# Kernel optimization log

Hardware: AMD Instinct MI355X
Metric: run time of the kernel (lower is better)

The kernel has to match this reference:

```python
import jax, jax.numpy as jnp
import numpy as np

EPS = 1e-6
NEG = -1e9
RES_RATIO = 1.0  # res_ratio init arg
MAKE_SYM = True


def _ln(x, g, b):
    m = jnp.mean(x, axis=-1, keepdims=True)
    v = jnp.mean((x - m) ** 2, axis=-1, keepdims=True)
    return (x - m) * jax.lax.rsqrt(v + EPS) * g + b


def _sim(q, k, W1q, W1k, b1, W2, b2):
    # NN(concat([q,k])) with first dense split into query/key halves:
    # relu(q@W1q + k@W1k + b1) @ W2 + b2  -> avoids materializing the 2d concat.
    qa = q @ W1q  # [b,n,sq,h]
    kb = k @ W1k  # [b,n,sk,h]
    h1 = jax.nn.relu(qa[:, :, :, None, :] + kb[:, :, None, :, :] + b1)  # [b,n,sq,sk,h]
    s = jnp.einsum('bnqkh,h->bnqk', h1, W2[:, 0]) + b2[0]
    if MAKE_SYM:
        qb = q @ W1k
        ka = k @ W1q
        h2 = jax.nn.relu(ka[:, :, None, :, :] + qb[:, :, :, None, :] + b1)
        s = s + jnp.einsum('bnqkh,h->bnqk', h2, W2[:, 0]) + b2[0]
    return s


def _attention(v, k, q, mask, Ww, bw, Wd, bd, W1q, W1k, b1, W2, b2):
    q = q @ Ww + bw
    k = k @ Ww + bw
    v = v @ Ww + bw
    logits = _sim(q, k, W1q, W1k, b1, W2, b2)
    if mask is not None:
        logits = logits + mask * NEG
    attn = jax.nn.softmax(logits, axis=-1)
    out = jnp.einsum('bnqk,bnkd->bnqd', attn, v)
    return out @ Wd + bd, attn


def setup_inputs() -> dict:
    key = jax.random.key(0)
    B, N, S, D, DFF, H = 4, 1, 256, 128, 512, 128
    ks = jax.random.split(key, 16)
    s = 0.02
    inp = {
        'x': jax.random.normal(ks[0], (B, N, S, D), jnp.float32),
        'enc_output': jax.random.normal(ks[1], (B, N, S, D), jnp.float32),
        'com_mask': jnp.zeros((B, N, S, S), jnp.float32),
        'dec_mask': jnp.zeros((B, N, S, S), jnp.float32),
        # shared pairwise-score MLP NN: Dense(H, relu) -> Dense(1)
        'W1q': jax.random.normal(ks[2], (D, H), jnp.float32) * s,
        'W1k': jax.random.normal(ks[3], (D, H), jnp.float32) * s,
        'b1': jnp.zeros((H,), jnp.float32),
        'W2': jax.random.normal(ks[4], (H, 1), jnp.float32) * s,
        'b2': jnp.zeros((1,), jnp.float32),
        # mha1 projections
        'Ww1': jax.random.normal(ks[5], (D, D), jnp.float32) * s,
        'bw1': jnp.zeros((D,), jnp.float32),
        'Wd1': jax.random.normal(ks[6], (D, D), jnp.float32) * s,
        'bd1': jnp.zeros((D,), jnp.float32),
        # mha2 projections
        'Ww2': jax.random.normal(ks[7], (D, D), jnp.float32) * s,
        'bw2': jnp.zeros((D,), jnp.float32),
        'Wd2': jax.random.normal(ks[8], (D, D), jnp.float32) * s,
        'bd2': jnp.zeros((D,), jnp.float32),
        # ffn
        'Wf1': jax.random.normal(ks[9], (D, DFF), jnp.float32) * s,
        'bf1': jnp.zeros((DFF,), jnp.float32),
        'Wf2': jax.random.normal(ks[10], (DFF, D), jnp.float32) * s,
        'bf2': jnp.zeros((D,), jnp.float32),
        # layernorms
        'ln1_g': jnp.ones((D,), jnp.float32), 'ln1_b': jnp.zeros((D,), jnp.float32),
        'ln2_g': jnp.ones((D,), jnp.float32), 'ln2_b': jnp.zeros((D,), jnp.float32),
        'ln3_g': jnp.ones((D,), jnp.float32), 'ln3_b': jnp.zeros((D,), jnp.float32),
    }
    return inp


def reference(x, enc_output, com_mask, dec_mask,
              W1q, W1k, b1, W2, b2,
              Ww1, bw1, Wd1, bd1,
              Ww2, bw2, Wd2, bd2,
              Wf1, bf1, Wf2, bf2,
              ln1_g, ln1_b, ln2_g, ln2_b, ln3_g, ln3_b):
    r = RES_RATIO
    # self-attention block (dropout inactive, eval mode)
    attn1, aw1 = _attention(x, x, x, com_mask, Ww1, bw1, Wd1, bd1, W1q, W1k, b1, W2, b2)
    out1 = _ln((2 - r) * attn1 + r * x, ln1_g, ln1_b)
    # cross-attention block
    attn2, aw2 = _attention(enc_output, enc_output, out1, dec_mask, Ww2, bw2, Wd2, bd2, W1q, W1k, b1, W2, b2)
    out2 = _ln((2 - r) * attn2 + r * out1, ln2_g, ln2_b)
    # ffn
    ffn = jax.nn.relu(out2 @ Wf1 + bf1) @ Wf2 + bf2
    out3 = _ln((2 - r) * ffn + r * out2, ln3_g, ln3_b)
    return out3
```

## Files before the change

kernel.cpp:

```cpp
#include <hip/hip_runtime.h>
#include <math.h>


#define LN_EPS 1e-6f
#define NEGV  (-1e9f)

constexpr int B = 4, S = 256, D = 128, H = 128, DFF = 512;
constexpr int R = B * S;

struct P {
    const float *x, *enc, *com_mask, *dec_mask;
    const float *W1q, *W1k, *b1, *W2;
    const float *Ww1, *bw1, *Wd1, *bd1;
    const float *Ww2, *bw2, *Wd2, *bd2;
    const float *Wf1, *bf1, *Wf2, *bf2;
    const float *ln1g, *ln1b, *ln2g, *ln2b, *ln3g, *ln3b;
    float *out;
    float *xw, *qa, *kb, *kv2w, *kb2, *ka2;
};

__global__ __launch_bounds__(512) void proj3_kernel(P p)
{
    const int g = blockIdx.y, tid = threadIdx.x;
    const int r0 = blockIdx.x * 8;
    __shared__ __align__(16) float Ash[8 * 128];
    __shared__ __align__(16) float Pw[8 * 128];
    __shared__ __align__(16) float Pp[2 * 8 * 128];

    const float* A    = g ? p.enc  : p.x;
    const float* Wp   = g ? p.Ww2  : p.Ww1;
    const float* bp   = g ? p.bw2  : p.bw1;
    float*       o_w  = g ? p.kv2w : p.xw;
    const float* Wsec = g ? p.W1k  : p.W1q;
    const float* bsec = g ? nullptr: p.b1;
    float*       o_s  = g ? p.kb2  : p.qa;
    const float* Wthr = g ? p.W1q  : p.W1k;
    float*       o_t  = g ? p.ka2  : p.kb;

    if (tid < 256)
        ((float4*)Ash)[tid] = ((const float4*)(A + (size_t)r0 * 128))[tid];
    __syncthreads();

    {
        const int kh = tid >> 8, unit = tid & 255, lr = unit >> 5, c4 = unit & 31;
        const float4* W4 = (const float4*)Wp;
        float4 acc = (kh == 0) ? ((const float4*)bp)[c4] : make_float4(0.f, 0.f, 0.f, 0.f);
        const int k0 = kh * 64;
        #pragma unroll 8
        for (int k = 0; k < 64; ++k) {
            const float a = Ash[lr * 128 + k0 + k];
            const float4 w = W4[(k0 + k) * 32 + c4];
            acc.x = fmaf(a, w.x, acc.x); acc.y = fmaf(a, w.y, acc.y);
            acc.z = fmaf(a, w.z, acc.z); acc.w = fmaf(a, w.w, acc.w);
        }
        ((float4*)Pp)[kh * 256 + unit] = acc;
    }
    __syncthreads();
    if (tid < 256) {
        const int lr = tid >> 5, c4 = tid & 31;
        const float4 a = ((const float4*)Pp)[tid];
        const float4 bq = ((const float4*)Pp)[256 + tid];
        const float4 w = make_float4(a.x + bq.x, a.y + bq.y, a.z + bq.z, a.w + bq.w);
        ((float4*)Pw)[tid] = w;
        ((float4*)o_w)[(size_t)(r0 + lr) * 32 + c4] = w;
    }
    __syncthreads();

    {
        const int which = tid >> 8, unit = tid & 255, lr = unit >> 5, c4 = unit & 31;
        const float* W = which ? Wthr : Wsec;
        const float* bb = which ? nullptr : bsec;
        float* o = which ? o_t : o_s;
        const float4* W4 = (const float4*)W;
        float4 acc = bb ? ((const float4*)bb)[c4] : make_float4(0.f, 0.f, 0.f, 0.f);
        #pragma unroll 8
        for (int k = 0; k < 128; ++k) {
            const float a = Pw[lr * 128 + k];
            const float4 w = W4[k * 32 + c4];
            acc.x = fmaf(a, w.x, acc.x); acc.y = fmaf(a, w.y, acc.y);
            acc.z = fmaf(a, w.z, acc.z); acc.w = fmaf(a, w.w, acc.w);
        }
        ((float4*)o)[(size_t)(r0 + lr) * 32 + c4] = acc;
    }
}

#define SC8(ACC, O1, X1, O2, X2)                                               \
    ACC = fmaf(fmaxf((O1).x + (X1).x, 0.f), w.x, ACC);                         \
    ACC = fmaf(fmaxf((O1).y + (X1).y, 0.f), w.y, ACC);                         \
    ACC = fmaf(fmaxf((O1).z + (X1).z, 0.f), w.z, ACC);                         \
    ACC = fmaf(fmaxf((O1).w + (X1).w, 0.f), w.w, ACC);                         \
    ACC = fmaf(fmaxf((O2).x + (X2).x, 0.f), w.x, ACC);                         \
    ACC = fmaf(fmaxf((O2).y + (X2).y, 0.f), w.y, ACC);                         \
    ACC = fmaf(fmaxf((O2).z + (X2).z, 0.f), w.z, ACC);                         \
    ACC = fmaf(fmaxf((O2).w + (X2).w, 0.f), w.w, ACC);

template<bool FIRST>
__device__ __forceinline__ void attn_stage(const P& p, float* smem,
                                           int tid, int r0, int bS)
{
    float* s8   = smem;
    float* rowS = smem + 1024;
    float* qa2L = smem + 18432;
    float* qb2L = smem + 18944;

    const float* __restrict__ S1g = FIRST ? p.kb : p.kb2;
    const float* __restrict__ S2g = FIRST ? p.qa : p.ka2;
    const float* mask = FIRST ? p.com_mask : p.dec_mask;
    const float* V    = FIRST ? p.xw : p.kv2w;
    const float* Wd   = FIRST ? p.Wd1 : p.Wd2;
    const float* bd   = FIRST ? p.bd1 : p.bd2;
    const float* lg   = FIRST ? p.ln1g : p.ln2g;
    const float* lb   = FIRST ? p.ln1b : p.ln2b;

    {
        const int hh = tid & 7, unit = tid >> 3, kk = unit & 31, rg = unit >> 5;
        const int rA = r0 + 2 * rg, rB = rA + 1;

        float4 o1A[4], o1B[4], o2A[4], o2B[4], w2r[4];
        #pragma unroll
        for (int j = 0; j < 4; ++j) {
            const int h = hh * 4 + 32 * j;
            if (FIRST) {
                o1A[j] = *(const float4*)(p.qa + (size_t)rA * H + h);
                o1B[j] = *(const float4*)(p.qa + (size_t)rB * H + h);
                o2A[j] = *(const float4*)(p.kb + (size_t)rA * H + h);
                o2B[j] = *(const float4*)(p.kb + (size_t)rB * H + h);
            } else {
                o1A[j] = *(const float4*)(qa2L + (2 * rg)     * H + h);
                o1B[j] = *(const float4*)(qa2L + (2 * rg + 1) * H + h);
                o2A[j] = *(const float4*)(qb2L + (2 * rg)     * H + h);
                o2B[j] = *(const float4*)(qb2L + (2 * rg + 1) * H + h);
            }
            w2r[j] = *(const float4*)(p.W2 + h);
        }

        for (int kt = 0; kt < 4; ++kt) {
            const float* __restrict__ r1a = S1g + (size_t)(bS + kt * 64 + kk)      * H;
            const float* __restrict__ r1b = S1g + (size_t)(bS + kt * 64 + kk + 32) * H;
            const float* __restrict__ r2a = S2g + (size_t)(bS + kt * 64 + kk)      * H;
            const float* __restrict__ r2b = S2g + (size_t)(bS + kt * 64 + kk + 32) * H;

            float4 x1a[4], x1b[4], x2a[4], x2b[4];
            #pragma unroll
            for (int j = 0; j < 4; ++j) {
                const int h = hh * 4 + 32 * j;
                x1a[j] = *(const float4*)(r1a + h);
                x1b[j] = *(const float4*)(r1b + h);
                x2a[j] = *(const float4*)(r2a + h);
                x2b[j] = *(const float4*)(r2b + h);
            }

            float aAa = 0.f, aAb = 0.f, aBa = 0.f, aBb = 0.f;
            #pragma unroll
            for (int j = 0; j < 4; ++j) {
                const float4 w = w2r[j];
                SC8(aAa, o1A[j], x1a[j], o2A[j], x2a[j])
                SC8(aAb, o1A[j], x1b[j], o2A[j], x2b[j])
                SC8(aBa, o1B[j], x1a[j], o2B[j], x2a[j])
                SC8(aBb, o1B[j], x1b[j], o2B[j], x2b[j])
            }
            #pragma unroll
            for (int o = 1; o < 8; o <<= 1) {
                aAa += __shfl_xor(aAa, o, 8);
                aAb += __shfl_xor(aAb, o, 8);
                aBa += __shfl_xor(aBa, o, 8);
                aBb += __shfl_xor(aBb, o, 8);
            }
            if (hh == 0) {
                const int kb0 = kt * 64;
                s8[(2 * rg)     * 256 + kb0 + kk]      = aAa;
                s8[(2 * rg)     * 256 + kb0 + kk + 32] = aAb;
                s8[(2 * rg + 1) * 256 + kb0 + kk]      = aBa;
                s8[(2 * rg + 1) * 256 + kb0 + kk + 32] = aBb;
            }
        }
    }
    __syncthreads();

    for (int i = tid; i < 1024; i += 512) {
        const int r = i >> 8, k = i & 255;
        s8[i] += mask[(size_t)(r0 + r) * S + k] * NEGV;
    }
    __syncthreads();

    {
        const int g = tid >> 6, c = tid & 63;
        if (g < 4) {
            float* rowp = s8 + g * 256;
            float m = -INFINITY;
            #pragma unroll
            for (int k = c; k < 256; k += 64) m = fmaxf(m, rowp[k]);
            for (int o = 32; o; o >>= 1) m = fmaxf(m, __shfl_xor(m, o, 64));
            float s = 0.f;
            #pragma unroll
            for (int k = c; k < 256; k += 64) { const float e = __expf(rowp[k] - m); rowp[k] = e; s += e; }
            for (int o = 32; o; o >>= 1) s += __shfl_xor(s, o, 64);
            const float rinv = 1.f / s;
            #pragma unroll
            for (int k = c; k < 256; k += 64) rowp[k] *= rinv;
        }
    }
    __syncthreads();

    float* avp = smem + 1536;
    float* aoS = smem + 3584;
    float* pp  = smem + 4096;

    {
        const int r = tid >> 7, t = tid & 127, kq = t >> 5, c4 = t & 31;
        const float4* V4 = (const float4*)(V + (size_t)bS * D);
        const float* sp = s8 + r * 256 + kq * 64;
        float4 acc = make_float4(0.f, 0.f, 0.f, 0.f);
        #pragma unroll 8
        for (int k = 0; k < 64; ++k) {
            const float a = sp[k];
            const float4 v = V4[(kq * 64 + k) * 32 + c4];
            acc.x = fmaf(a, v.x, acc.x); acc.y = fmaf(a, v.y, acc.y);
            acc.z = fmaf(a, v.z, acc.z); acc.w = fmaf(a, v.w, acc.w);
        }
        ((float4*)avp)[(r * 4 + kq) * 32 + c4] = acc;
    }
    __syncthreads();
    if (tid < 128) {
        const int r = tid >> 5, c4 = tid & 31;
        float4 s0 = ((const float4*)avp)[(r * 4 + 0) * 32 + c4];
        const float4 s1 = ((const float4*)avp)[(r * 4 + 1) * 32 + c4];
        const float4 s2 = ((const float4*)avp)[(r * 4 + 2) * 32 + c4];
        const float4 s3 = ((const float4*)avp)[(r * 4 + 3) * 32 + c4];
        s0.x += s1.x + s2.x + s3.x; s0.y += s1.y + s2.y + s3.y;
        s0.z += s1.z + s2.z + s3.z; s0.w += s1.w + s2.w + s3.w;
        ((float4*)aoS)[r * 32 + c4] = s0;
    }
    __syncthreads();

    {
        const int kq = tid >> 7, unit = tid & 127, r = unit >> 5, c4 = unit & 31;
        const float4* W4 = (const float4*)Wd;
        const float* ap = aoS + r * 128 + kq * 32;
        float4 acc = make_float4(0.f, 0.f, 0.f, 0.f);
        #pragma unroll 8
        for (int k = 0; k < 32; ++k) {
            const float a = ap[k];
            const float4 w = W4[(kq * 32 + k) * 32 + c4];
            acc.x = fmaf(a, w.x, acc.x); acc.y = fmaf(a, w.y, acc.y);
            acc.z = fmaf(a, w.z, acc.z); acc.w = fmaf(a, w.w, acc.w);
        }
        ((float4*)pp)[kq * 128 + unit] = acc;
    }
    __syncthreads();

    if (tid < 128) {
        const int r = tid >> 5, c4 = tid & 31;
        const float4 p0 = ((const float4*)pp)[tid];
        const float4 p1 = ((const float4*)pp)[128 + tid];
        const float4 p2 = ((const float4*)pp)[256 + tid];
        const float4 p3 = ((const float4*)pp)[384 + tid];
        const float4 bv0 = ((const float4*)bd)[c4];
        float4 r4;
        if (FIRST) r4 = ((const float4*)(p.x + (size_t)(r0 + r) * 128))[c4];
        else       r4 = ((const float4*)rowS)[r * 32 + c4];
        const float x0 = p0.x + p1.x + p2.x + p3.x + bv0.x + r4.x;
        const float x1 = p0.y + p1.y + p2.y + p3.y + bv0.y + r4.y;
        const float x2 = p0.z + p1.z + p2.z + p3.z + bv0.z + r4.z;
        const float x3 = p0.w + p1.w + p2.w + p3.w + bv0.w + r4.w;
        float s  = x0 + x1 + x2 + x3;
        float s2 = x0 * x0 + x1 * x1 + x2 * x2 + x3 * x3;
        for (int o = 16; o; o >>= 1) { s += __shfl_xor(s, o, 32); s2 += __shfl_xor(s2, o, 32); }
        const float m = s * (1.f / 128), var = s2 * (1.f / 128) - m * m;
        const float rs = rsqrtf(var + LN_EPS);
        const float4 gv = ((const float4*)lg)[c4], bv = ((const float4*)lb)[c4];
        float4 o4;
        o4.x = (x0 - m) * rs * gv.x + bv.x; o4.y = (x1 - m) * rs * gv.y + bv.y;
        o4.z = (x2 - m) * rs * gv.z + bv.z; o4.w = (x3 - m) * rs * gv.w + bv.w;
        ((float4*)rowS)[r * 32 + c4] = o4;
    }
    __syncthreads();

    if (FIRST) {
        float* qpp  = smem + 6144;
        float* q2wS = smem + 8192;
        float* qp2  = smem + 8704;
        {
            const int kq = tid >> 7, unit = tid & 127, r = unit >> 5, c4 = unit & 31;
            const float4* W4 = (const float4*)p.Ww2;
            const float* ap = rowS + r * 128 + kq * 32;
            float4 acc = make_float4(0.f, 0.f, 0.f, 0.f);
            #pragma unroll 8
            for (int k = 0; k < 32; ++k) {
                const float a = ap[k];
                const float4 w = W4[(kq * 32 + k) * 32 + c4];
                acc.x = fmaf(a, w.x, acc.x); acc.y = fmaf(a, w.y, acc.y);
                acc.z = fmaf(a, w.z, acc.z); acc.w = fmaf(a, w.w, acc.w);
            }
            ((float4*)qpp)[kq * 128 + unit] = acc;
        }
        __syncthreads();
        if (tid < 128) {
            const int c4 = tid & 31;
            const float4 p0 = ((const float4*)qpp)[tid];
            const float4 p1 = ((const float4*)qpp)[128 + tid];
            const float4 p2 = ((const float4*)qpp)[256 + tid];
            const float4 p3 = ((const float4*)qpp)[384 + tid];
            const float4 bw = ((const float4*)p.bw2)[c4];
            ((float4*)q2wS)[tid] = make_float4(p0.x + p1.x + p2.x + p3.x + bw.x,
                                               p0.y + p1.y + p2.y + p3.y + bw.y,
                                               p0.z + p1.z + p2.z + p3.z + bw.z,
                                               p0.w + p1.w + p2.w + p3.w + bw.w);
        }
        __syncthreads();
        {
            const int which = tid >> 8, sub = tid & 255;
            const int kh = sub >> 7, unit2 = sub & 127;
            const float4* W4 = (const float4*)(which ? p.W1k : p.W1q);
            const int r = unit2 >> 5;
            const float* ap = q2wS + r * 128 + kh * 64;
            float4 acc = make_float4(0.f, 0.f, 0.f, 0.f);
            #pragma unroll 8
            for (int k = 0; k < 64; ++k) {
                const float a = ap[k];
                const float4 w = W4[(kh * 64 + k) * 32 + (unit2 & 31)];
                acc.x = fmaf(a, w.x, acc.x); acc.y = fmaf(a, w.y, acc.y);
                acc.z = fmaf(a, w.z, acc.z); acc.w = fmaf(a, w.w, acc.w);
            }
            ((float4*)qp2)[(which * 2 + kh) * 128 + unit2] = acc;
        }
        __syncthreads();
        if (tid < 256) {
            const int which = tid >> 7, unit2 = tid & 127;
            const int c4 = unit2 & 31;
            const float4 p0 = ((const float4*)qp2)[(which * 2 + 0) * 128 + unit2];
            const float4 p1 = ((const float4*)qp2)[(which * 2 + 1) * 128 + unit2];
            const float4 b1v = ((const float4*)p.b1)[c4];
            float* oq = which ? qb2L : qa2L;
            ((float4*)oq)[unit2] =
                make_float4(p0.x + p1.x + b1v.x, p0.y + p1.y + b1v.y,
                            p0.z + p1.z + b1v.z, p0.w + p1.w + b1v.w);
        }
        __syncthreads();
    } else {
        float* hidP = smem + 1536;
        float* part = smem + 9984;
        {
            const int c = tid & 127, kh = tid >> 7;
            const float4* Wf1_4 = (const float4*)p.Wf1;
            float4 a0 = make_float4(0.f,0.f,0.f,0.f), a1 = a0, a2 = a0, a3 = a0;
            const int kbase = kh * 32;
            #pragma unroll 8
            for (int k = 0; k < 32; ++k) {
                const int kk = kbase + k;
                const float4 w = Wf1_4[kk * 128 + c];
                const float s0 = rowS[kk],       s1 = rowS[128 + kk];
                const float s2 = rowS[256 + kk], s3 = rowS[384 + kk];
                a0.x=fmaf(s0,w.x,a0.x); a0.y=fmaf(s0,w.y,a0.y); a0.z=fmaf(s0,w.z,a0.z); a0.w=fmaf(s0,w.w,a0.w);
                a1.x=fmaf(s1,w.x,a1.x); a1.y=fmaf(s1,w.y,a1.y); a1.z=fmaf(s1,w.z,a1.z); a1.w=fmaf(s1,w.w,a1.w);
                a2.x=fmaf(s2,w.x,a2.x); a2.y=fmaf(s2,w.y,a2.y); a2.z=fmaf(s2,w.z,a2.z); a2.w=fmaf(s2,w.w,a2.w);
                a3.x=fmaf(s3,w.x,a3.x); a3.y=fmaf(s3,w.y,a3.y); a3.z=fmaf(s3,w.z,a3.z); a3.w=fmaf(s3,w.w,a3.w);
            }
            float4* h4 = (float4*)hidP;
            const int base = kh * 512;
            h4[base + 0*128 + c] = a0; h4[base + 1*128 + c] = a1;
            h4[base + 2*128 + c] = a2; h4[base + 3*128 + c] = a3;
        }
        __syncthreads();
        for (int i = tid; i < 2048; i += 512) {
            hidP[i] = fmaxf(hidP[i] + hidP[2048 + i] + hidP[4096 + i] + hidP[6144 + i]
                            + p.bf1[i & 511], 0.f);
        }
        __syncthreads();
        {
            const int c4f = tid & 31, kg = tid >> 5;
            const float4* Wf2_4 = (const float4*)p.Wf2;
            float4 a0 = make_float4(0.f,0.f,0.f,0.f), a1 = a0, a2 = a0, a3 = a0;
            const int kbase = kg * 32;
            const float* h0 = hidP + 0 * 512 + kbase;
            const float* h1 = hidP + 1 * 512 + kbase;
            const float* h2 = hidP + 2 * 512 + kbase;
            const float* h3 = hidP + 3 * 512 + kbase;
            #pragma unroll 8
            for (int k = 0; k < 32; ++k) {
                const float4 w = Wf2_4[(kbase + k) * 32 + c4f];
                const float s0 = h0[k], s1 = h1[k], s2 = h2[k], s3 = h3[k];
                a0.x=fmaf(s0,w.x,a0.x); a0.y=fmaf(s0,w.y,a0.y); a0.z=fmaf(s0,w.z,a0.z); a0.w=fmaf(s0,w.w,a0.w);
                a1.x=fmaf(s1,w.x,a1.x); a1.y=fmaf(s1,w.y,a1.y); a1.z=fmaf(s1,w.z,a1.z); a1.w=fmaf(s1,w.w,a1.w);
                a2.x=fmaf(s2,w.x,a2.x); a2.y=fmaf(s2,w.y,a2.y); a2.z=fmaf(s2,w.z,a2.z); a2.w=fmaf(s2,w.w,a2.w);
                a3.x=fmaf(s3,w.x,a3.x); a3.y=fmaf(s3,w.y,a3.y); a3.z=fmaf(s3,w.z,a3.z); a3.w=fmaf(s3,w.w,a3.w);
            }
            float4* p4 = (float4*)part;
            p4[kg * 128 + 0 * 32 + c4f] = a0; p4[kg * 128 + 1 * 32 + c4f] = a1;
            p4[kg * 128 + 2 * 32 + c4f] = a2; p4[kg * 128 + 3 * 32 + c4f] = a3;
        }
        __syncthreads();
        if (tid < 128) {
            const int r = tid >> 5, c4 = tid & 31;
            const float4* p4 = (const float4*)part;
            float4 sum = ((const float4*)p.bf2)[c4];
            #pragma unroll
            for (int kg = 0; kg < 16; ++kg) {
                const float4 v = p4[kg * 128 + r * 32 + c4];
                sum.x += v.x; sum.y += v.y; sum.z += v.z; sum.w += v.w;
            }
            const float4 r4 = ((const float4*)rowS)[r * 32 + c4];
            const float x0 = sum.x + r4.x, x1 = sum.y + r4.y;
            const float x2 = sum.z + r4.z, x3 = sum.w + r4.w;
            float s  = x0 + x1 + x2 + x3;
            float s2 = x0 * x0 + x1 * x1 + x2 * x2 + x3 * x3;
            for (int o = 16; o; o >>= 1) { s += __shfl_xor(s, o, 32); s2 += __shfl_xor(s2, o, 32); }
            const float m = s * (1.f / 128), var = s2 * (1.f / 128) - m * m;
            const float rs = rsqrtf(var + LN_EPS);
            const float4 gv = ((const float4*)p.ln3g)[c4], bv = ((const float4*)p.ln3b)[c4];
            float4 o4;
            o4.x = (x0 - m) * rs * gv.x + bv.x; o4.y = (x1 - m) * rs * gv.y + bv.y;
            o4.z = (x2 - m) * rs * gv.z + bv.z; o4.w = (x3 - m) * rs * gv.w + bv.w;
            ((float4*)p.out)[(size_t)(r0 + r) * 32 + c4] = o4;
        }
    }
}

__global__ __launch_bounds__(512) void fused_attn12_kernel(P p)
{
    __shared__ __align__(16) float smem[19456];
    const int tid = threadIdx.x;
    const int r0 = blockIdx.x * 4, bS = (r0 >> 8) * S;
    attn_stage<true >(p, smem, tid, r0, bS);
    attn_stage<false>(p, smem, tid, r0, bS);
}

extern "C" void kernel_launch(void* const* d_in, const int* in_sizes, int n_in,
                              void* d_out, int out_size, void* d_ws, size_t ws_size,
                              hipStream_t stream) {
    (void)in_sizes; (void)n_in; (void)out_size; (void)ws_size;
    P p;
    p.x        = (const float*)d_in[0];
    p.enc      = (const float*)d_in[1];
    p.com_mask = (const float*)d_in[2];
    p.dec_mask = (const float*)d_in[3];
    p.W1q = (const float*)d_in[4];
    p.W1k = (const float*)d_in[5];
    p.b1  = (const float*)d_in[6];
    p.W2  = (const float*)d_in[7];
    p.Ww1 = (const float*)d_in[9];
    p.bw1 = (const float*)d_in[10];
    p.Wd1 = (const float*)d_in[11];
    p.bd1 = (const float*)d_in[12];
    p.Ww2 = (const float*)d_in[13];
    p.bw2 = (const float*)d_in[14];
    p.Wd2 = (const float*)d_in[15];
    p.bd2 = (const float*)d_in[16];
    p.Wf1 = (const float*)d_in[17];
    p.bf1 = (const float*)d_in[18];
    p.Wf2 = (const float*)d_in[19];
    p.bf2 = (const float*)d_in[20];
    p.ln1g = (const float*)d_in[21];
    p.ln1b = (const float*)d_in[22];
    p.ln2g = (const float*)d_in[23];
    p.ln2b = (const float*)d_in[24];
    p.ln3g = (const float*)d_in[25];
    p.ln3b = (const float*)d_in[26];
    p.out  = (float*)d_out;

    float* ws = (float*)d_ws;
    const size_t RD = (size_t)R * D;
    p.xw    = ws;
    p.qa    = p.xw    + RD;
    p.kb    = p.qa    + RD;
    p.kv2w  = p.kb    + RD;
    p.kb2   = p.kv2w  + RD;
    p.ka2   = p.kb2   + RD;

    proj3_kernel<<<dim3(R / 8, 2), 512, 0, stream>>>(p);
    fused_attn12_kernel<<<R / 4, 512, 0, stream>>>(p);
}
```

Before: 164.5 us.

## Split projection K-loops, double-buffer key loads, fold mask and softmax normalization

The projection kernel now handles 4 rows per block with a 4-way and then a 2-way split-K and shared-memory reductions, so it launches twice as many blocks and each thread runs a shorter serial loop. In the attention stage, key-side rows are double-buffered in registers so the next tile's global loads are issued while the current tile is being computed. The mask add moves into the score write, which removes one pass over shared memory and a barrier. Softmax normalization is deferred to the attention-output reduction through a per-row reciprocal, and the shared-memory layout is compacted. The cost is more registers for the double buffers and extra barriers in the projection kernel.

```diff
diff --git a/kernel.cpp b/kernel.cpp
--- a/kernel.cpp
+++ b/kernel.cpp
@@ -22,10 +22,11 @@
 __global__ __launch_bounds__(512) void proj3_kernel(P p)
 {
     const int g = blockIdx.y, tid = threadIdx.x;
-    const int r0 = blockIdx.x * 8;
-    __shared__ __align__(16) float Ash[8 * 128];
-    __shared__ __align__(16) float Pw[8 * 128];
-    __shared__ __align__(16) float Pp[2 * 8 * 128];
+    const int r0 = blockIdx.x * 4;
+    __shared__ __align__(16) float Ash[4 * 128];
+    __shared__ __align__(16) float Pw[4 * 128];
+    __shared__ __align__(16) float Pp[4 * 4 * 128];
+    __shared__ __align__(16) float P2[2 * 2 * 4 * 128];
 
     const float* A    = g ? p.enc  : p.x;
     const float* Wp   = g ? p.Ww2  : p.Ww1;
@@ -37,50 +38,67 @@
     const float* Wthr = g ? p.W1q  : p.W1k;
     float*       o_t  = g ? p.ka2  : p.kb;
 
-    if (tid < 256)
+    if (tid < 128)
         ((float4*)Ash)[tid] = ((const float4*)(A + (size_t)r0 * 128))[tid];
     __syncthreads();
 
     {
-        const int kh = tid >> 8, unit = tid & 255, lr = unit >> 5, c4 = unit & 31;
+        const int kh = tid >> 7, unit = tid & 127, lr = unit >> 5, c4 = unit & 31;
         const float4* W4 = (const float4*)Wp;
         float4 acc = (kh == 0) ? ((const float4*)bp)[c4] : make_float4(0.f, 0.f, 0.f, 0.f);
-        const int k0 = kh * 64;
+        const int k0 = kh * 32;
         #pragma unroll 8
-        for (int k = 0; k < 64; ++k) {
+        for (int k = 0; k < 32; ++k) {
             const float a = Ash[lr * 128 + k0 + k];
             const float4 w = W4[(k0 + k) * 32 + c4];
             acc.x = fmaf(a, w.x, acc.x); acc.y = fmaf(a, w.y, acc.y);
             acc.z = fmaf(a, w.z, acc.z); acc.w = fmaf(a, w.w, acc.w);
         }
-        ((float4*)Pp)[kh * 256 + unit] = acc;
-    }
-    __syncthreads();
-    if (tid < 256) {
+        ((float4*)Pp)[kh * 128 + unit] = acc;
+    }
+    __syncthreads();
+    if (tid < 128) {
         const int lr = tid >> 5, c4 = tid & 31;
-        const float4 a = ((const float4*)Pp)[tid];
-        const float4 bq = ((const float4*)Pp)[256 + tid];
-        const float4 w = make_float4(a.x + bq.x, a.y + bq.y, a.z + bq.z, a.w + bq.w);
+        const float4 a0 = ((const float4*)Pp)[tid];
+        const float4 a1 = ((const float4*)Pp)[128 + tid];
+        const float4 a2 = ((const float4*)Pp)[256 + tid];
+        const float4 a3 = ((const float4*)Pp)[384 + tid];
+        const float4 w = make_float4(a0.x + a1.x + a2.x + a3.x,
+                                     a0.y + a1.y + a2.y + a3.y,
+                                     a0.z + a1.z + a2.z + a3.z,
+                                     a0.w + a1.w + a2.w + a3.w);
         ((float4*)Pw)[tid] = w;
         ((float4*)o_w)[(size_t)(r0 + lr) * 32 + c4] = w;
     }
     __syncthreads();
 
     {
-        const int which = tid >> 8, unit = tid & 255, lr = unit >> 5, c4 = unit & 31;
+        const int which = tid >> 8, sub = tid & 255;
+        const int kh = sub >> 7, unit2 = sub & 127, lr = unit2 >> 5, c4 = unit2 & 31;
         const float* W = which ? Wthr : Wsec;
         const float* bb = which ? nullptr : bsec;
-        float* o = which ? o_t : o_s;
         const float4* W4 = (const float4*)W;
-        float4 acc = bb ? ((const float4*)bb)[c4] : make_float4(0.f, 0.f, 0.f, 0.f);
+        float4 acc = (kh == 0 && bb) ? ((const float4*)bb)[c4]
+                                     : make_float4(0.f, 0.f, 0.f, 0.f);
+        const int k0 = kh * 64;
         #pragma unroll 8
-        for (int k = 0; k < 128; ++k) {
-            const float a = Pw[lr * 128 + k];
-            const float4 w = W4[k * 32 + c4];
+        for (int k = 0; k < 64; ++k) {
+            const float a = Pw[lr * 128 + k0 + k];
+            const float4 w = W4[(k0 + k) * 32 + c4];
             acc.x = fmaf(a, w.x, acc.x); acc.y = fmaf(a, w.y, acc.y);
             acc.z = fmaf(a, w.z, acc.z); acc.w = fmaf(a, w.w, acc.w);
         }
-        ((float4*)o)[(size_t)(r0 + lr) * 32 + c4] = acc;
+        ((float4*)P2)[(which * 2 + kh) * 128 + unit2] = acc;
+    }
+    __syncthreads();
+    if (tid < 256) {
+        const int which = tid >> 7, unit2 = tid & 127;
+        const int lr = unit2 >> 5, c4 = unit2 & 31;
+        const float4 p0 = ((const float4*)P2)[(which * 2 + 0) * 128 + unit2];
+        const float4 p1 = ((const float4*)P2)[(which * 2 + 1) * 128 + unit2];
+        float* o = which ? o_t : o_s;
+        ((float4*)o)[(size_t)(r0 + lr) * 32 + c4] =
+            make_float4(p0.x + p1.x, p0.y + p1.y, p0.z + p1.z, p0.w + p1.w);
     }
 }
 
@@ -94,14 +112,32 @@
     ACC = fmaf(fmaxf((O2).z + (X2).z, 0.f), w.z, ACC);                         \
     ACC = fmaf(fmaxf((O2).w + (X2).w, 0.f), w.w, ACC);
 
+#define LOADK(BUF, KT)                                                         \
+    {                                                                          \
+        const float* r1a_ = S1g + (size_t)(bS + (KT) * 64 + kk) * H;           \
+        const float* r1b_ = S1g + (size_t)(bS + (KT) * 64 + kk + 32) * H;      \
+        const float* r2a_ = S2g + (size_t)(bS + (KT) * 64 + kk) * H;           \
+        const float* r2b_ = S2g + (size_t)(bS + (KT) * 64 + kk + 32) * H;      \
+        _Pragma("unroll")                                                      \
+        for (int j = 0; j < 4; ++j) {                                          \
+            const int h = hh * 4 + 32 * j;                                     \
+            X1a[BUF][j] = *(const float4*)(r1a_ + h);                          \
+            X1b[BUF][j] = *(const float4*)(r1b_ + h);                          \
+            X2a[BUF][j] = *(const float4*)(r2a_ + h);                          \
+            X2b[BUF][j] = *(const float4*)(r2b_ + h);                          \
+        }                                                                      \
+    }
+
 template<bool FIRST>
 __device__ __forceinline__ void attn_stage(const P& p, float* smem,
                                            int tid, int r0, int bS)
 {
-    float* s8   = smem;
-    float* rowS = smem + 1024;
-    float* qa2L = smem + 18432;
-    float* qb2L = smem + 18944;
+    float* s8    = smem;
+    float* rowS  = smem + 1024;
+    float* rinvS = smem + 1536;
+    float* qa2L  = smem + 1552;
+    float* qb2L  = smem + 2064;
+    constexpr int SB = 2576;
 
     const float* __restrict__ S1g = FIRST ? p.kb : p.kb2;
     const float* __restrict__ S2g = FIRST ? p.qa : p.ka2;
@@ -126,38 +162,28 @@
                 o2A[j] = *(const float4*)(p.kb + (size_t)rA * H + h);
                 o2B[j] = *(const float4*)(p.kb + (size_t)rB * H + h);
             } else {
-                o1A[j] = *(const float4*)(qa2L + (2 * rg)     * H + h);
+                o1A[j] = *(const float4*)(qa2L + (2 * rg) * H + h);
                 o1B[j] = *(const float4*)(qa2L + (2 * rg + 1) * H + h);
-                o2A[j] = *(const float4*)(qb2L + (2 * rg)     * H + h);
+                o2A[j] = *(const float4*)(qb2L + (2 * rg) * H + h);
                 o2B[j] = *(const float4*)(qb2L + (2 * rg + 1) * H + h);
             }
             w2r[j] = *(const float4*)(p.W2 + h);
         }
 
+        float4 X1a[2][4], X1b[2][4], X2a[2][4], X2b[2][4];
+        LOADK(0, 0)
+        #pragma unroll
         for (int kt = 0; kt < 4; ++kt) {
-            const float* __restrict__ r1a = S1g + (size_t)(bS + kt * 64 + kk)      * H;
-            const float* __restrict__ r1b = S1g + (size_t)(bS + kt * 64 + kk + 32) * H;
-            const float* __restrict__ r2a = S2g + (size_t)(bS + kt * 64 + kk)      * H;
-            const float* __restrict__ r2b = S2g + (size_t)(bS + kt * 64 + kk + 32) * H;
-
-            float4 x1a[4], x1b[4], x2a[4], x2b[4];
-            #pragma unroll
-            for (int j = 0; j < 4; ++j) {
-                const int h = hh * 4 + 32 * j;
-                x1a[j] = *(const float4*)(r1a + h);
-                x1b[j] = *(const float4*)(r1b + h);
-                x2a[j] = *(const float4*)(r2a + h);
-                x2b[j] = *(const float4*)(r2b + h);
-            }
-
+            const int cur = kt & 1;
+            if (kt < 3) LOADK(cur ^ 1, kt + 1)
             float aAa = 0.f, aAb = 0.f, aBa = 0.f, aBb = 0.f;
             #pragma unroll
             for (int j = 0; j < 4; ++j) {
                 const float4 w = w2r[j];
-                SC8(aAa, o1A[j], x1a[j], o2A[j], x2a[j])
-                SC8(aAb, o1A[j], x1b[j], o2A[j], x2b[j])
-                SC8(aBa, o1B[j], x1a[j], o2B[j], x2a[j])
-                SC8(aBb, o1B[j], x1b[j], o2B[j], x2b[j])
+                SC8(aAa, o1A[j], X1a[cur][j], o2A[j], X2a[cur][j])
+                SC8(aAb, o1A[j], X1b[cur][j], o2A[j], X2b[cur][j])
+                SC8(aBa, o1B[j], X1a[cur][j], o2B[j], X2a[cur][j])
+                SC8(aBb, o1B[j], X1b[cur][j], o2B[j], X2b[cur][j])
             }
             #pragma unroll
             for (int o = 1; o < 8; o <<= 1) {
@@ -167,19 +193,13 @@
                 aBb += __shfl_xor(aBb, o, 8);
             }
             if (hh == 0) {
-                const int kb0 = kt * 64;
-                s8[(2 * rg)     * 256 + kb0 + kk]      = aAa;
-                s8[(2 * rg)     * 256 + kb0 + kk + 32] = aAb;
-                s8[(2 * rg + 1) * 256 + kb0 + kk]      = aBa;
-                s8[(2 * rg + 1) * 256 + kb0 + kk + 32] = aBb;
-            }
-        }
-    }
-    __syncthreads();
-
-    for (int i = tid; i < 1024; i += 512) {
-        const int r = i >> 8, k = i & 255;
-        s8[i] += mask[(size_t)(r0 + r) * S + k] * NEGV;
+                const int k = kt * 64 + kk;
+                s8[(2 * rg) * 256 + k]          = aAa + mask[(size_t)rA * S + k] * NEGV;
+                s8[(2 * rg) * 256 + k + 32]     = aAb + mask[(size_t)rA * S + k + 32] * NEGV;
+                s8[(2 * rg + 1) * 256 + k]      = aBa + mask[(size_t)rB * S + k] * NEGV;
+                s8[(2 * rg + 1) * 256 + k + 32] = aBb + mask[(size_t)rB * S + k + 32] * NEGV;
+            }
+        }
     }
     __syncthreads();
 
@@ -195,16 +215,14 @@
             #pragma unroll
             for (int k = c; k < 256; k += 64) { const float e = __expf(rowp[k] - m); rowp[k] = e; s += e; }
             for (int o = 32; o; o >>= 1) s += __shfl_xor(s, o, 64);
-            const float rinv = 1.f / s;
-            #pragma unroll
-            for (int k = c; k < 256; k += 64) rowp[k] *= rinv;
-        }
-    }
-    __syncthreads();
-
-    float* avp = smem + 1536;
-    float* aoS = smem + 3584;
-    float* pp  = smem + 4096;
+            if (c == 0) rinvS[g] = 1.f / s;
+        }
+    }
+    __syncthreads();
+
+    float* avp = smem + SB;
+    float* aoS = smem + SB + 2048;
+    float* pp  = smem + SB + 2560;
 
     {
         const int r = tid >> 7, t = tid & 127, kq = t >> 5, c4 = t & 31;
@@ -227,9 +245,10 @@
         const float4 s1 = ((const float4*)avp)[(r * 4 + 1) * 32 + c4];
         const float4 s2 = ((const float4*)avp)[(r * 4 + 2) * 32 + c4];
         const float4 s3 = ((const float4*)avp)[(r * 4 + 3) * 32 + c4];
-        s0.x += s1.x + s2.x + s3.x; s0.y += s1.y + s2.y + s3.y;
-        s0.z += s1.z + s2.z + s3.z; s0.w += s1.w + s2.w + s3.w;
-        ((float4*)aoS)[r * 32 + c4] = s0;
+        const float rv = rinvS[r];
+        ((float4*)aoS)[r * 32 + c4] = make_float4(
+            (s0.x + s1.x + s2.x + s3.x) * rv, (s0.y + s1.y + s2.y + s3.y) * rv,
+            (s0.z + s1.z + s2.z + s3.z) * rv, (s0.w + s1.w + s2.w + s3.w) * rv);
     }
     __syncthreads();
 
@@ -277,9 +296,9 @@
     __syncthreads();
 
     if (FIRST) {
-        float* qpp  = smem + 6144;
-        float* q2wS = smem + 8192;
-        float* qp2  = smem + 8704;
+        float* qpp  = smem + SB;
+        float* q2wS = smem + SB + 2048;
+        float* qp2  = smem + SB + 2560;
         {
             const int kq = tid >> 7, unit = tid & 127, r = unit >> 5, c4 = unit & 31;
             const float4* W4 = (const float4*)p.Ww2;
@@ -338,8 +357,8 @@
         }
         __syncthreads();
     } else {
-        float* hidP = smem + 1536;
-        float* part = smem + 9984;
+        float* hidP = smem + SB;
+        float* part = smem + SB + 8192;
         {
             const int c = tid & 127, kh = tid >> 7;
             const float4* Wf1_4 = (const float4*)p.Wf1;
@@ -418,7 +437,7 @@
 
 __global__ __launch_bounds__(512) void fused_attn12_kernel(P p)
 {
-    __shared__ __align__(16) float smem[19456];
+    __shared__ __align__(16) float smem[18960];
     const int tid = threadIdx.x;
     const int r0 = blockIdx.x * 4, bS = (r0 >> 8) * S;
     attn_stage<true >(p, smem, tid, r0, bS);
@@ -467,6 +486,6 @@
     p.kb2   = p.kv2w  + RD;
     p.ka2   = p.kb2   + RD;
 
-    proj3_kernel<<<dim3(R / 8, 2), 512, 0, stream>>>(p);
+    proj3_kernel<<<dim3(R / 4, 2), 512, 0, stream>>>(p);
     fused_attn12_kernel<<<R / 4, 512, 0, stream>>>(p);
 }
```

New measurement: 168.8 us. 2.6% more time.
